# Optimization experiments

Hardware: AMD Instinct MI355X
Metric: run time of the kernel (lower is better)

Reference implementation:

```python
import jax, jax.numpy as jnp
import numpy as np

FORCE = 8.0
N_STATE = 40
BATCH = 524288


def setup_inputs() -> dict:
    key = jax.random.key(0)
    x0 = jax.random.normal(key, (BATCH, N_STATE), dtype=jnp.float32)
    t = jnp.float32(0.0)          # unused: system is autonomous (torch code passes nan)
    dt = jnp.float32(0.05)        # canonical Lorenz96 RK4 step
    return {"x0": x0, "t": t, "dt": dt}


def _dxdt(x):
    # torch shift(x, n) == roll(x, -n, dims=-1)
    # dxdt = (shift(x,1) - shift(x,-2)) * shift(x,-1) - x + force
    return (jnp.roll(x, -1, axis=-1) - jnp.roll(x, 2, axis=-1)) * jnp.roll(x, 1, axis=-1) - x + FORCE


def reference(x0, t, dt):
    # Classic RK4 step (rk4_torch); t is ignored (autonomous RHS).
    k1 = _dxdt(x0)
    k2 = _dxdt(x0 + 0.5 * dt * k1)
    k3 = _dxdt(x0 + 0.5 * dt * k2)
    k4 = _dxdt(x0 + dt * k3)
    return x0 + (dt / 6.0) * (k1 + 2.0 * k2 + 2.0 * k3 + k4)
```

## Files before the change

kernel.cpp:

```cpp
#include <hip/hip_runtime.h>


#define FORCE 8.0f

__device__ __forceinline__ float4 rk4_chunk(const float4 vm2, const float4 vm1,
                                            const float4 v0,  const float4 vp1,
                                            const float dt,   const float hdt)
{
    float xa[16];
    xa[0]=vm2.x;  xa[1]=vm2.y;  xa[2]=vm2.z;  xa[3]=vm2.w;
    xa[4]=vm1.x;  xa[5]=vm1.y;  xa[6]=vm1.z;  xa[7]=vm1.w;
    xa[8]=v0.x;   xa[9]=v0.y;   xa[10]=v0.z;  xa[11]=v0.w;
    xa[12]=vp1.x; xa[13]=vp1.y; xa[14]=vp1.z; xa[15]=vp1.w;

    float k1[13], y1[13];
#pragma unroll
    for (int i = 0; i < 13; ++i)
        k1[i] = (xa[i+3] - xa[i]) * xa[i+1] - xa[i+2] + FORCE;
#pragma unroll
    for (int i = 0; i < 13; ++i)
        y1[i] = fmaf(hdt, k1[i], xa[i+2]);

    float k2[10], y2[10];
#pragma unroll
    for (int i = 0; i < 10; ++i)
        k2[i] = (y1[i+3] - y1[i]) * y1[i+1] - y1[i+2] + FORCE;
#pragma unroll
    for (int i = 0; i < 10; ++i)
        y2[i] = fmaf(hdt, k2[i], xa[i+4]);

    float k3[7], y3[7];
#pragma unroll
    for (int i = 0; i < 7; ++i)
        k3[i] = (y2[i+3] - y2[i]) * y2[i+1] - y2[i+2] + FORCE;
#pragma unroll
    for (int i = 0; i < 7; ++i)
        y3[i] = fmaf(dt, k3[i], xa[i+6]);

    float k4[4];
#pragma unroll
    for (int i = 0; i < 4; ++i)
        k4[i] = (y3[i+3] - y3[i]) * y3[i+1] - y3[i+2] + FORCE;

    const float sc = dt * (1.0f / 6.0f);
    float4 r;
    {
        float t0 = k1[6] + k4[0]; t0 = fmaf(2.0f, k2[4], t0); t0 = fmaf(2.0f, k3[2], t0);
        float t1 = k1[7] + k4[1]; t1 = fmaf(2.0f, k2[5], t1); t1 = fmaf(2.0f, k3[3], t1);
        float t2 = k1[8] + k4[2]; t2 = fmaf(2.0f, k2[6], t2); t2 = fmaf(2.0f, k3[4], t2);
        float t3 = k1[9] + k4[3]; t3 = fmaf(2.0f, k2[7], t3); t3 = fmaf(2.0f, k3[5], t3);
        r.x = fmaf(sc, t0, xa[8]);
        r.y = fmaf(sc, t1, xa[9]);
        r.z = fmaf(sc, t2, xa[10]);
        r.w = fmaf(sc, t3, xa[11]);
    }
    return r;
}

__global__ __launch_bounds__(256)
void lorenz96_rk4_halo4(const float4* __restrict__ x0,
                        const float* __restrict__ dt_p,
                        float4* __restrict__ out,
                        unsigned nf4)
{
    const unsigned tid  = blockIdx.x * blockDim.x + threadIdx.x;
    const unsigned w    = tid >> 6;
    const unsigned lane = tid & 63u;
    const unsigned fb   = w * 256u + lane;

    const float dt  = dt_p[0];
    const float hdt = 0.5f * dt;

    float4 a0_, a1_, a2_, a3_;
    float4 b0_, b1_, b2_, b3_;
    float4 c0_, c1_, c2_, c3_;
    float4 d0_, d1_, d2_, d3_;
    unsigned f0_, f1_, f2_, f3_;
    bool act0, act1, act2, act3;

#define LOADC(J, A, B, C, D, F, ACT)                                         \
    {                                                                        \
        F = fb + 64u * (J);                                                  \
        ACT = (F < nf4);                                                     \
        if (ACT) {                                                           \
            const unsigned r  = F / 10u;                                     \
            const unsigned c  = F - r * 10u;                                 \
            const unsigned rb = r * 10u;                                     \
            const unsigned cm2 = (c >= 2u) ? c - 2u : c + 8u;                \
            const unsigned cm1 = (c >= 1u) ? c - 1u : c + 9u;                \
            const unsigned cp1 = (c <= 8u) ? c + 1u : c - 9u;                \
            A = x0[rb + cm2];                                                \
            B = x0[rb + cm1];                                                \
            C = x0[rb + c  ];                                                \
            D = x0[rb + cp1];                                                \
        }                                                                    \
    }

#define COMPC(A, B, C, D, F, ACT)                                            \
    if (ACT) { out[F] = rk4_chunk(A, B, C, D, dt, hdt); }

    LOADC(0, a0_, b0_, c0_, d0_, f0_, act0)
    LOADC(1, a1_, b1_, c1_, d1_, f1_, act1)
    LOADC(2, a2_, b2_, c2_, d2_, f2_, act2)
    COMPC(a0_, b0_, c0_, d0_, f0_, act0)
    LOADC(3, a3_, b3_, c3_, d3_, f3_, act3)
    COMPC(a1_, b1_, c1_, d1_, f1_, act1)
    COMPC(a2_, b2_, c2_, d2_, f2_, act2)
    COMPC(a3_, b3_, c3_, d3_, f3_, act3)

#undef LOADC
#undef COMPC
}

extern "C" void kernel_launch(void* const* d_in, const int* in_sizes, int n_in,
                              void* d_out, int out_size, void* d_ws, size_t ws_size,
                              hipStream_t stream) {
    const float4* x0 = (const float4*)d_in[0];
    const float* dt = (const float*)d_in[2];
    float4* out = (float4*)d_out;

    const unsigned nf4 = (unsigned)((long)in_sizes[0] / 4);
    const unsigned nwaves = (nf4 + 255u) / 256u;
    const int block = 256;
    const unsigned grid = (nwaves + 3u) / 4u;
    lorenz96_rk4_halo4<<<dim3(grid), dim3(block), 0, stream>>>(x0, dt, out, nf4);
}
```

Measured before the change: 151.2 us.

## Switch to persistent grid-stride kernel with double-buffered loads

```diff
diff --git a/kernel.cpp b/kernel.cpp
--- a/kernel.cpp
+++ b/kernel.cpp
@@ -44,72 +44,69 @@
 
     const float sc = dt * (1.0f / 6.0f);
     float4 r;
-    {
-        float t0 = k1[6] + k4[0]; t0 = fmaf(2.0f, k2[4], t0); t0 = fmaf(2.0f, k3[2], t0);
-        float t1 = k1[7] + k4[1]; t1 = fmaf(2.0f, k2[5], t1); t1 = fmaf(2.0f, k3[3], t1);
-        float t2 = k1[8] + k4[2]; t2 = fmaf(2.0f, k2[6], t2); t2 = fmaf(2.0f, k3[4], t2);
-        float t3 = k1[9] + k4[3]; t3 = fmaf(2.0f, k2[7], t3); t3 = fmaf(2.0f, k3[5], t3);
-        r.x = fmaf(sc, t0, xa[8]);
-        r.y = fmaf(sc, t1, xa[9]);
-        r.z = fmaf(sc, t2, xa[10]);
-        r.w = fmaf(sc, t3, xa[11]);
-    }
+    float t0 = k1[6] + k4[0]; t0 = fmaf(2.0f, k2[4], t0); t0 = fmaf(2.0f, k3[2], t0);
+    float t1 = k1[7] + k4[1]; t1 = fmaf(2.0f, k2[5], t1); t1 = fmaf(2.0f, k3[3], t1);
+    float t2 = k1[8] + k4[2]; t2 = fmaf(2.0f, k2[6], t2); t2 = fmaf(2.0f, k3[4], t2);
+    float t3 = k1[9] + k4[3]; t3 = fmaf(2.0f, k2[7], t3); t3 = fmaf(2.0f, k3[5], t3);
+    r.x = fmaf(sc, t0, xa[8]);
+    r.y = fmaf(sc, t1, xa[9]);
+    r.z = fmaf(sc, t2, xa[10]);
+    r.w = fmaf(sc, t3, xa[11]);
     return r;
 }
 
 __global__ __launch_bounds__(256)
-void lorenz96_rk4_halo4(const float4* __restrict__ x0,
-                        const float* __restrict__ dt_p,
-                        float4* __restrict__ out,
-                        unsigned nf4)
+void lorenz96_rk4_persist(const float4* __restrict__ x0,
+                          const float* __restrict__ dt_p,
+                          float4* __restrict__ out,
+                          unsigned nf4,
+                          unsigned stride,
+                          int cstep,
+                          int niter)
 {
-    const unsigned tid  = blockIdx.x * blockDim.x + threadIdx.x;
-    const unsigned w    = tid >> 6;
-    const unsigned lane = tid & 63u;
-    const unsigned fb   = w * 256u + lane;
+    const unsigned tid = blockIdx.x * blockDim.x + threadIdx.x;
 
     const float dt  = dt_p[0];
     const float hdt = 0.5f * dt;
 
-    float4 a0_, a1_, a2_, a3_;
-    float4 b0_, b1_, b2_, b3_;
-    float4 c0_, c1_, c2_, c3_;
-    float4 d0_, d1_, d2_, d3_;
-    unsigned f0_, f1_, f2_, f3_;
-    bool act0, act1, act2, act3;
+    float4 A0, B0, C0, D0;
+    float4 A1, B1, C1, D1;
 
-#define LOADC(J, A, B, C, D, F, ACT)                                         \
+#define LOADS(F, C, A, B, Cc, D)                                             \
     {                                                                        \
-        F = fb + 64u * (J);                                                  \
-        ACT = (F < nf4);                                                     \
-        if (ACT) {                                                           \
-            const unsigned r  = F / 10u;                                     \
-            const unsigned c  = F - r * 10u;                                 \
-            const unsigned rb = r * 10u;                                     \
-            const unsigned cm2 = (c >= 2u) ? c - 2u : c + 8u;                \
-            const unsigned cm1 = (c >= 1u) ? c - 1u : c + 9u;                \
-            const unsigned cp1 = (c <= 8u) ? c + 1u : c - 9u;                \
-            A = x0[rb + cm2];                                                \
-            B = x0[rb + cm1];                                                \
-            C = x0[rb + c  ];                                                \
-            D = x0[rb + cp1];                                                \
-        }                                                                    \
+        const int om2 = ((C) >= 2) ? -2 : 8;                                 \
+        const int om1 = ((C) >= 1) ? -1 : 9;                                 \
+        const int op1 = ((C) <= 8) ?  1 : -9;                                \
+        A  = x0[(F) + om2];                                                  \
+        B  = x0[(F) + om1];                                                  \
+        Cc = x0[(F)];                                                        \
+        D  = x0[(F) + op1];                                                  \
     }
 
-#define COMPC(A, B, C, D, F, ACT)                                            \
-    if (ACT) { out[F] = rk4_chunk(A, B, C, D, dt, hdt); }
+    unsigned f0 = tid;
+    int      c0 = (int)(f0 % 10u);
+    bool   act0 = (f0 < nf4);
+    if (act0) LOADS(f0, c0, A0, B0, C0, D0)
 
-    LOADC(0, a0_, b0_, c0_, d0_, f0_, act0)
-    LOADC(1, a1_, b1_, c1_, d1_, f1_, act1)
-    LOADC(2, a2_, b2_, c2_, d2_, f2_, act2)
-    COMPC(a0_, b0_, c0_, d0_, f0_, act0)
-    LOADC(3, a3_, b3_, c3_, d3_, f3_, act3)
-    COMPC(a1_, b1_, c1_, d1_, f1_, act1)
-    COMPC(a2_, b2_, c2_, d2_, f2_, act2)
-    COMPC(a3_, b3_, c3_, d3_, f3_, act3)
+    unsigned f1 = f0 + stride;
+    int      c1 = c0 + cstep; if (c1 >= 10) c1 -= 10;
 
-#undef LOADC
-#undef COMPC
+    for (int it = 0; it < niter; it += 2) {
+        const bool act1 = (f1 < nf4);
+        if (act1) LOADS(f1, c1, A1, B1, C1, D1)
+        if (act0) out[f0] = rk4_chunk(A0, B0, C0, D0, dt, hdt);
+
+        f0 = f1 + stride;
+        c0 = c1 + cstep; if (c0 >= 10) c0 -= 10;
+        act0 = (f0 < nf4);
+
+        if (act0) LOADS(f0, c0, A0, B0, C0, D0)
+        if (act1) out[f1] = rk4_chunk(A1, B1, C1, D1, dt, hdt);
+
+        f1 = f0 + stride;
+        c1 = c0 + cstep; if (c1 >= 10) c1 -= 10;
+    }
+#undef LOADS
 }
 
 extern "C" void kernel_launch(void* const* d_in, const int* in_sizes, int n_in,
@@ -120,8 +117,12 @@
     float4* out = (float4*)d_out;
 
     const unsigned nf4 = (unsigned)((long)in_sizes[0] / 4);
-    const unsigned nwaves = (nf4 + 255u) / 256u;
     const int block = 256;
-    const unsigned grid = (nwaves + 3u) / 4u;
-    lorenz96_rk4_halo4<<<dim3(grid), dim3(block), 0, stream>>>(x0, dt, out, nf4);
+    const unsigned grid = 2048;
+    const unsigned stride = grid * block;
+    const int cstep = (int)(stride % 10u);
+    int niter = (int)((nf4 + stride - 1) / stride);
+    if (niter & 1) ++niter;
+    lorenz96_rk4_persist<<<dim3(grid), dim3(block), 0, stream>>>(
+        x0, dt, out, nf4, stride, cstep, niter);
 }
```

Result: slower. 154.3 us (+2.1%).
